# Optimization experiments

Hardware: AMD Instinct MI355X
Metric: run time of the kernel (lower is better)

Reference implementation:

```python
import jax, jax.numpy as jnp
import numpy as np

IN_CH = 4
OUT_CH = 64
T = 100            # max points per pillar
P_MAX = 12000      # max pillars
DX = 0.16
DY = 0.16
XMIN, YMIN, ZMIN, XMAX, YMAX, ZMAX = -40.0, -40.0, -3.0, 40.0, 40.0, 1.0
NX = int(round((XMAX - XMIN) / DX))   # 500
NY = int(round((YMAX - YMIN) / DY))   # 500
EPS = 1e-5
B, N = 2, 120000


def setup_inputs() -> dict:
    key = jax.random.key(0)
    ks = jax.random.split(key, 8)
    # realistic LiDAR-like cloud: x,y spread over the grid, z mostly in range
    xy = jax.random.normal(ks[0], (B, N, 2)) * 15.0
    z = jax.random.uniform(ks[1], (B, N, 1), minval=-3.2, maxval=1.2)
    inten = jax.random.uniform(ks[2], (B, N, 1))
    points = jnp.concatenate([xy, z, inten], axis=-1)

    def bn_params(k):
        k1, k2, k3, k4 = jax.random.split(k, 4)
        g = 1.0 + 0.1 * jax.random.normal(k1, (OUT_CH,))
        b = 0.1 * jax.random.normal(k2, (OUT_CH,))
        m = 0.1 * jax.random.normal(k3, (OUT_CH,))
        v = 0.5 + jax.random.uniform(k4, (OUT_CH,))
        return g, b, m, v

    w1 = jax.random.normal(ks[3], (OUT_CH, IN_CH + 4)) * 0.3
    w2 = jax.random.normal(ks[4], (OUT_CH, OUT_CH)) * 0.1
    g1, b1, m1, v1 = bn_params(ks[5])
    g2, b2, m2, v2 = bn_params(ks[6])
    return dict(points=points, w1=w1, g1=g1, b1=b1, m1=m1, v1=v1,
                w2=w2, g2=g2, b2=b2, m2=m2, v2=v2)


def _pillarize(pts):
    # pts: [N, 4] -> dense pillar tensor [P_MAX, T, 8], validity mask, pillar keys
    x, y, z = pts[:, 0], pts[:, 1], pts[:, 2]
    valid = (x >= XMIN) & (x < XMAX) & (y >= YMIN) & (y < YMAX) & (z >= ZMIN) & (z < ZMAX)
    xi = jnp.clip(jnp.floor((x - XMIN) / DX), 0, NX - 1).astype(jnp.int32)
    yi = jnp.clip(jnp.floor((y - YMIN) / DY), 0, NY - 1).astype(jnp.int32)
    big = jnp.int32(NX * NY)  # sentinel key for invalid points (sorts last)
    keyv = jnp.where(valid, xi * NY + yi, big)
    order = jnp.argsort(keyv)          # stable sort == torch.unique ordering
    sk = keyv[order]
    ps = pts[order]
    vs = sk < big
    n = pts.shape[0]
    idx = jnp.arange(n, dtype=jnp.int32)
    new = vs & jnp.concatenate([jnp.ones((1,), bool), sk[1:] != sk[:-1]])
    rank = jnp.cumsum(new.astype(jnp.int32)) - 1          # dense pillar id (sorted)
    p_eff = jnp.minimum(jnp.sum(new.astype(jnp.int32)), P_MAX)
    start = jax.lax.cummax(jnp.where(new, idx, jnp.int32(-1)))
    intra = idx - start                                   # slot within pillar
    keep = vs & (rank < P_MAX) & (intra < T)
    r = jnp.where(keep, rank, P_MAX)
    t = jnp.where(keep, intra, T)
    pillar_pts = jnp.zeros((P_MAX, T, IN_CH), pts.dtype).at[r, t].set(ps, mode='drop')
    keys = jnp.zeros((P_MAX,), jnp.int32).at[r].set(sk, mode='drop')
    pvalid = jnp.arange(P_MAX, dtype=jnp.int32) < p_eff
    xi_u = (keys // NY).astype(pts.dtype)
    yi_u = (keys % NY).astype(pts.dtype)
    xc = xi_u * DX + XMIN + DX / 2
    yc = yi_u * DY + YMIN + DY / 2
    # enhanced features are computed for ALL T slots (incl. empty), like the original
    x_off = pillar_pts[:, :, 0] - xc[:, None]
    y_off = pillar_pts[:, :, 1] - yc[:, None]
    xc_t = jnp.broadcast_to(xc[:, None], (P_MAX, T))
    yc_t = jnp.broadcast_to(yc[:, None], (P_MAX, T))
    enh = jnp.stack([xc_t, yc_t, x_off, y_off], axis=-1)
    pin = jnp.concatenate([pillar_pts, enh], axis=-1)     # [P_MAX, T, 8]
    return pin, pvalid, keys


def _forward(points, w1, g1, b1, m1, v1, w2, g2, b2, m2, v2):
    pin, pvalid, keys = jax.vmap(_pillarize)(points)      # [B, P_MAX, T, 8]

    def bn(h, g, b, m, v):
        return (h - m) * (g * jax.lax.rsqrt(v + EPS)) + b

    h = jax.nn.relu(bn(jnp.einsum('bptc,oc->bpto', pin, w1), g1, b1, m1, v1))
    h = jax.nn.relu(bn(jnp.einsum('bptc,oc->bpto', h, w2), g2, b2, m2, v2))
    feats = jnp.max(h, axis=2)                            # max-pool over T
    feats = jnp.where(pvalid[..., None], feats, 0.0)      # zero-pad unused pillars
    bidx = jnp.broadcast_to(jnp.arange(points.shape[0], dtype=jnp.int32)[:, None], pvalid.shape)
    xi_u = jnp.where(pvalid, keys // NY, 0)
    yi_u = jnp.where(pvalid, keys % NY, 0)
    coords = jnp.stack([bidx, xi_u, yi_u], axis=-1)       # [B, P_MAX, 3]
    return feats, coords


def reference(points, w1, g1, b1, m1, v1, w2, g2, b2, m2, v2):
    return _forward(points, w1, g1, b1, m1, v1, w2, g2, b2, m2, v2)
```

## Files before the change

kernel.cpp:

```cpp
#include <hip/hip_runtime.h>
#include <stdint.h>
#include <stddef.h>

#define NBATCH 2
#define NPTS   120000
#define T_SLOTS 100
#define PMAX   12000
#define NXG    500
#define NYG    500
#define NBINS  (NXG*NYG)
#define NCH    ((NBINS + 63)/64)
#define NG     ((NCH + 63)/64)

#define FEAT_BLOCKS 6000

#define WS_FLAGS   ((size_t)0)
#define WS_SLOT    (WS_FLAGS + (size_t)NBATCH*NBINS)
#define WS_ZEROEND (WS_SLOT  + (size_t)NBATCH*PMAX*4)
#define WS_MASKS   (WS_ZEROEND)
#define WS_PDAT    (WS_MASKS + (size_t)NBATCH*NCH*8)
#define WS_CHOFF   (WS_PDAT  + (size_t)NBATCH*PMAX*T_SLOTS*16)
#define WS_PILKEY  (WS_CHOFF + (size_t)NBATCH*NCH*4)
#define WS_GRPS    (WS_PILKEY+ (size_t)NBATCH*PMAX*4)
#define WS_PTOT    (WS_GRPS  + (size_t)NBATCH*NG*4)
#define WS_NEEDED  (WS_PTOT  + (size_t)NBATCH*4)

#define ZERO_F4    (WS_ZEROEND / 16)


__global__ void k_zero(float4* __restrict__ dst) {
    int i = blockIdx.x * blockDim.x + threadIdx.x;
    if (i < (int)ZERO_F4) {
        float4 z; z.x = 0.0f; z.y = 0.0f; z.z = 0.0f; z.w = 0.0f;
        dst[i] = z;
    }
}

__global__ void k_key(const float4* __restrict__ pts4,
                      unsigned char* __restrict__ flags) {
    int i = blockIdx.x * blockDim.x + threadIdx.x;
    if (i >= NBATCH * NPTS) return;
    int b = i / NPTS;
    float4 P = pts4[i];
    float x = P.x, y = P.y, z = P.z;
    bool valid = (x >= -40.0f) && (x < 40.0f) &&
                 (y >= -40.0f) && (y < 40.0f) &&
                 (z >= -3.0f)  && (z < 1.0f);
    if (valid) {
        float fx = floorf((x + 40.0f) / 0.16f);
        float fy = floorf((y + 40.0f) / 0.16f);
        fx = fminf(fmaxf(fx, 0.0f), (float)(NXG - 1));
        fy = fminf(fmaxf(fy, 0.0f), (float)(NYG - 1));
        int key = (int)fx * NYG + (int)fy;
        flags[(size_t)b * NBINS + key] = 1;
    }
}

__global__ __launch_bounds__(1024)
void k_scanA(const unsigned char* __restrict__ flags,
             unsigned long long* __restrict__ masks,
             int* __restrict__ grpsum) {
    __shared__ int scnt[64];
    const int g    = blockIdx.x;
    const int b    = blockIdx.y;
    const int tid  = threadIdx.x;
    const int lane = tid & 63;
    const int w    = tid >> 6;
    const unsigned char* fb = flags + (size_t)b * NBINS;

    #pragma unroll
    for (int q = 0; q < 4; ++q) {
        int chl = w * 4 + q;
        int ch  = g * 64 + chl;
        int bin = ch * 64 + lane;
        int pres = (ch < NCH && bin < NBINS && fb[bin]) ? 1 : 0;
        unsigned long long m = __ballot(pres);
        if (lane == 0) {
            if (ch < NCH) masks[(size_t)b * NCH + ch] = m;
            scnt[chl] = __popcll(m);
        }
    }
    __syncthreads();
    if (w == 0) {
        int v = scnt[lane];
        #pragma unroll
        for (int off = 32; off > 0; off >>= 1) v += __shfl_xor(v, off);
        if (lane == 0) grpsum[b * NG + g] = v;
    }
}

__global__ void k_choff(const unsigned long long* __restrict__ masks,
                        const int* __restrict__ grpsum,
                        int* __restrict__ choff, int* __restrict__ ptot) {
    int tid  = threadIdx.x;
    int lane = tid & 63;
    int gw   = blockIdx.x * 4 + (tid >> 6);
    if (gw >= NBATCH * NG) return;
    int b = gw / NG, g = gw - b * NG;

    int gs = (lane < NG) ? grpsum[b * NG + lane] : 0;
    int incl = gs;
    #pragma unroll
    for (int off = 1; off < 64; off <<= 1) {
        int t2 = __shfl_up(incl, off);
        if (lane >= off) incl += t2;
    }
    int tot  = __shfl(incl, NG - 1);
    int goff = __shfl(incl, (g == 0) ? 0 : g - 1);
    if (g == 0) goff = 0;
    if (g == 0 && lane == 0) ptot[b] = tot;

    int ch = g * 64 + lane;
    int cs = (ch < NCH) ? __popcll(masks[(size_t)b * NCH + ch]) : 0;
    int incl2 = cs;
    #pragma unroll
    for (int off = 1; off < 64; off <<= 1) {
        int t2 = __shfl_up(incl2, off);
        if (lane >= off) incl2 += t2;
    }
    if (ch < NCH) choff[(size_t)b * NCH + ch] = goff + incl2 - cs;
}

__global__ void k_fill(const float4* __restrict__ pts4,
                       const unsigned long long* __restrict__ masks,
                       const int* __restrict__ choff, int* __restrict__ slotctr,
                       int* __restrict__ pilkey, float4* __restrict__ pdat) {
    int i = blockIdx.x * blockDim.x + threadIdx.x;
    if (i >= NBATCH * NPTS) return;
    int b = i / NPTS;
    float4 P = pts4[i];
    float x = P.x, y = P.y, z = P.z;
    bool valid = (x >= -40.0f) && (x < 40.0f) &&
                 (y >= -40.0f) && (y < 40.0f) &&
                 (z >= -3.0f)  && (z < 1.0f);
    if (!valid) return;
    float fx = floorf((x + 40.0f) / 0.16f);
    float fy = floorf((y + 40.0f) / 0.16f);
    fx = fminf(fmaxf(fx, 0.0f), (float)(NXG - 1));
    fy = fminf(fmaxf(fy, 0.0f), (float)(NYG - 1));
    int key = (int)fx * NYG + (int)fy;

    int ch = key >> 6;
    unsigned long long m = masks[(size_t)b * NCH + ch];
    int r = choff[(size_t)b * NCH + ch] +
            __popcll(m & ((1ULL << (key & 63)) - 1ULL));
    if (r >= PMAX) return;
    pilkey[b * PMAX + r] = key;
    int t = atomicAdd(&slotctr[b * PMAX + r], 1);
    if (t < T_SLOTS)
        pdat[((size_t)(b * PMAX + r)) * T_SLOTS + t] = P;
}

__global__ __launch_bounds__(256, 8)
void k_feats(const float4* __restrict__ pdat,
             const float* __restrict__ w1, const float* __restrict__ g1,
             const float* __restrict__ b1, const float* __restrict__ m1,
             const float* __restrict__ v1,
             const float* __restrict__ w2, const float* __restrict__ g2,
             const float* __restrict__ b2, const float* __restrict__ m2,
             const float* __restrict__ v2,
             const int* __restrict__ pilkey, const int* __restrict__ slotctr,
             const int* __restrict__ ptot, float* __restrict__ out) {
    __shared__ float4 w2s[16 * 64];
    __shared__ __align__(16) float h1s[4][64];

    const int tid  = threadIdx.x;
    const int lane = tid & 63;
    const int widx = tid >> 6;
    const int o = lane;

    float* feats  = out;
    float* coords = out + (size_t)NBATCH * PMAX * 64;

    const int p = blockIdx.x * 4 + widx;
    const int b = p / PMAX;
    const int r = p - b * PMAX;

    const float4* prow = pdat + (size_t)p * T_SLOTS;
    int key = pilkey[p];
    int c   = slotctr[p];
    int pe = ptot[b]; if (pe > PMAX) pe = PMAX;

    float s1 = g1[o] * rsqrtf(v1[o] + 1e-5f);
    float b1f = b1[o] - m1[o] * s1;
    float w1r[8];
    {
        const float4* w14 = (const float4*)(w1 + o * 8);
        float4 a = w14[0], c4 = w14[1];
        w1r[0] = a.x * s1;  w1r[1] = a.y * s1;  w1r[2] = a.z * s1;  w1r[3] = a.w * s1;
        w1r[4] = c4.x * s1; w1r[5] = c4.y * s1; w1r[6] = c4.z * s1; w1r[7] = c4.w * s1;
    }
    float wx = w1r[0] + w1r[6];
    float wy = w1r[1] + w1r[7];

    float s2 = g2[o] * rsqrtf(v2[o] + 1e-5f);
    float b2f = b2[o] - m2[o] * s2;
    {
        const float4* w2row = (const float4*)(w2 + o * 64);
        #pragma unroll
        for (int it = 0; it < 4; ++it) {
            int kq = widx + it * 4;
            float4 t = w2row[kq];
            t.x *= s2; t.y *= s2; t.z *= s2; t.w *= s2;
            w2s[kq * 64 + o] = t;
        }
    }
    __syncthreads();

    size_t frow = (size_t)p * 64;
    size_t crow = (size_t)p * 3;

    if (r >= pe) {
        feats[frow + o] = 0.0f;
        if (o < 3) coords[crow + o] = (o == 0) ? (float)b : 0.0f;
        return;
    }

    int xi = key / NYG;
    int yi = key - xi * NYG;
    float xc = (float)xi * 0.16f - 40.0f + 0.08f;
    float yc = (float)yi * 0.16f - 40.0f + 0.08f;

    float pb = b1f + (w1r[4] - w1r[6]) * xc + (w1r[5] - w1r[7]) * yc;

    int pc = (c < T_SLOTS) ? c : T_SLOTS;
    int nIter = pc + ((c < T_SLOTS) ? 1 : 0);

    float acc = 0.0f;
    for (int s = 0; s < nIter; ++s) {
        float4 P;
        if (s < pc) {
            P = prow[s];
        } else {
            P.x = 0.0f; P.y = 0.0f; P.z = 0.0f; P.w = 0.0f;
        }
        float h = pb;
        h += wx * P.x; h += wy * P.y;
        h += w1r[2] * P.z; h += w1r[3] * P.w;
        h = fmaxf(h, 0.0f);

        h1s[widx][o] = h;
        asm volatile("s_waitcnt lgkmcnt(0)" ::: "memory");

        float a0 = b2f, a1 = 0.0f, a2 = 0.0f, a3 = 0.0f;
        #pragma unroll
        for (int kq = 0; kq < 16; ++kq) {
            float4 w  = w2s[kq * 64 + o];
            float4 hb = *(const float4*)&h1s[widx][kq * 4];
            a0 += w.x * hb.x; a1 += w.y * hb.y;
            a2 += w.z * hb.z; a3 += w.w * hb.w;
        }
        float h2 = fmaxf((a0 + a1) + (a2 + a3), 0.0f);
        acc = fmaxf(acc, h2);
    }

    feats[frow + o] = acc;
    if (o < 3)
        coords[crow + o] = (o == 0) ? (float)b : ((o == 1) ? (float)xi : (float)yi);
}


extern "C" void kernel_launch(void* const* d_in, const int* in_sizes, int n_in,
                              void* d_out, int out_size, void* d_ws, size_t ws_size,
                              hipStream_t stream) {
    if (ws_size < WS_NEEDED) return;

    const float4* pts4 = (const float4*)d_in[0];
    const float* w1  = (const float*)d_in[1];
    const float* g1  = (const float*)d_in[2];
    const float* b1  = (const float*)d_in[3];
    const float* m1  = (const float*)d_in[4];
    const float* v1  = (const float*)d_in[5];
    const float* w2  = (const float*)d_in[6];
    const float* g2  = (const float*)d_in[7];
    const float* b2  = (const float*)d_in[8];
    const float* m2  = (const float*)d_in[9];
    const float* v2  = (const float*)d_in[10];

    char* ws = (char*)d_ws;
    unsigned char* flags = (unsigned char*)(ws + WS_FLAGS);
    int*  slotctr = (int*)(ws + WS_SLOT);
    unsigned long long* masks = (unsigned long long*)(ws + WS_MASKS);
    float4* pdat  = (float4*)(ws + WS_PDAT);
    int*  choff   = (int*)(ws + WS_CHOFF);
    int*  pilkey  = (int*)(ws + WS_PILKEY);
    int*  grpsum  = (int*)(ws + WS_GRPS);
    int*  ptot    = (int*)(ws + WS_PTOT);
    float* out    = (float*)d_out;

    dim3 blk256(256);
    int npt = NBATCH * NPTS;
    dim3 grdPts((npt + 255) / 256);

    hipLaunchKernelGGL(k_zero, dim3((ZERO_F4 + 255) / 256), blk256, 0, stream,
                       (float4*)(ws + WS_FLAGS));

    hipLaunchKernelGGL(k_key, grdPts, blk256, 0, stream, pts4, flags);

    hipLaunchKernelGGL(k_scanA, dim3(NG, NBATCH), dim3(1024), 0, stream,
                       flags, masks, grpsum);

    hipLaunchKernelGGL(k_choff, dim3((NBATCH * NG + 3) / 4), blk256, 0, stream,
                       masks, grpsum, choff, ptot);

    hipLaunchKernelGGL(k_fill, grdPts, blk256, 0, stream,
                       pts4, masks, choff, slotctr, pilkey, pdat);

    hipLaunchKernelGGL(k_feats, dim3(FEAT_BLOCKS), blk256, 0, stream,
                       pdat, w1, g1, b1, m1, v1, w2, g2, b2, m2, v2,
                       pilkey, slotctr, ptot, out);
}
```

Before: 48.16 us.

## Process two batch pillars per wavefront to reuse shared weight loads

Each wavefront now handles pillar r from both batches at once. Every w2 row read from shared memory is reused for two hidden vectors, and half as many blocks are launched, so each block's weight setup in LDS is paid once per pair of pillars. The cost is loop divergence when the two pillars have different point counts, extra registers, and the dot product regrouped into two accumulators instead of four, which lengthens the dependency chains.

```diff
diff --git a/kernel.cpp b/kernel.cpp
--- a/kernel.cpp
+++ b/kernel.cpp
@@ -12,7 +12,7 @@
 #define NCH    ((NBINS + 63)/64)
 #define NG     ((NCH + 63)/64)
 
-#define FEAT_BLOCKS 6000
+#define FEAT_BLOCKS 3000
 
 #define WS_FLAGS   ((size_t)0)
 #define WS_SLOT    (WS_FLAGS + (size_t)NBATCH*NBINS)
@@ -162,7 +162,7 @@
              const int* __restrict__ pilkey, const int* __restrict__ slotctr,
              const int* __restrict__ ptot, float* __restrict__ out) {
     __shared__ float4 w2s[16 * 64];
-    __shared__ __align__(16) float h1s[4][64];
+    __shared__ __align__(16) float h1s[4][2][64];
 
     const int tid  = threadIdx.x;
     const int lane = tid & 63;
@@ -172,14 +172,16 @@
     float* feats  = out;
     float* coords = out + (size_t)NBATCH * PMAX * 64;
 
-    const int p = blockIdx.x * 4 + widx;
-    const int b = p / PMAX;
-    const int r = p - b * PMAX;
-
-    const float4* prow = pdat + (size_t)p * T_SLOTS;
-    int key = pilkey[p];
-    int c   = slotctr[p];
-    int pe = ptot[b]; if (pe > PMAX) pe = PMAX;
+    const int r  = blockIdx.x * 4 + widx;
+    const int pA = r;
+    const int pB = r + PMAX;
+
+    const float4* prowA = pdat + (size_t)pA * T_SLOTS;
+    const float4* prowB = pdat + (size_t)pB * T_SLOTS;
+    int keyA = pilkey[pA], keyB = pilkey[pB];
+    int cA   = slotctr[pA], cB = slotctr[pB];
+    int pe0 = ptot[0]; if (pe0 > PMAX) pe0 = PMAX;
+    int pe1 = ptot[1]; if (pe1 > PMAX) pe1 = PMAX;
 
     float s1 = g1[o] * rsqrtf(v1[o] + 1e-5f);
     float b1f = b1[o] - m1[o] * s1;
@@ -207,56 +209,71 @@
     }
     __syncthreads();
 
-    size_t frow = (size_t)p * 64;
-    size_t crow = (size_t)p * 3;
-
-    if (r >= pe) {
-        feats[frow + o] = 0.0f;
-        if (o < 3) coords[crow + o] = (o == 0) ? (float)b : 0.0f;
-        return;
-    }
-
-    int xi = key / NYG;
-    int yi = key - xi * NYG;
-    float xc = (float)xi * 0.16f - 40.0f + 0.08f;
-    float yc = (float)yi * 0.16f - 40.0f + 0.08f;
-
-    float pb = b1f + (w1r[4] - w1r[6]) * xc + (w1r[5] - w1r[7]) * yc;
-
-    int pc = (c < T_SLOTS) ? c : T_SLOTS;
-    int nIter = pc + ((c < T_SLOTS) ? 1 : 0);
-
-    float acc = 0.0f;
-    for (int s = 0; s < nIter; ++s) {
-        float4 P;
-        if (s < pc) {
-            P = prow[s];
-        } else {
-            P.x = 0.0f; P.y = 0.0f; P.z = 0.0f; P.w = 0.0f;
-        }
-        float h = pb;
-        h += wx * P.x; h += wy * P.y;
-        h += w1r[2] * P.z; h += w1r[3] * P.w;
-        h = fmaxf(h, 0.0f);
-
-        h1s[widx][o] = h;
+    int xiA = keyA / NYG, yiA = keyA - xiA * NYG;
+    int xiB = keyB / NYG, yiB = keyB - xiB * NYG;
+    float xcA = (float)xiA * 0.16f - 40.0f + 0.08f;
+    float ycA = (float)yiA * 0.16f - 40.0f + 0.08f;
+    float xcB = (float)xiB * 0.16f - 40.0f + 0.08f;
+    float ycB = (float)yiB * 0.16f - 40.0f + 0.08f;
+    float pbA = b1f + (w1r[4] - w1r[6]) * xcA + (w1r[5] - w1r[7]) * ycA;
+    float pbB = b1f + (w1r[4] - w1r[6]) * xcB + (w1r[5] - w1r[7]) * ycB;
+
+    bool liveA = (r < pe0), liveB = (r < pe1);
+    int pcA = liveA ? ((cA < T_SLOTS) ? cA : T_SLOTS) : 0;
+    int pcB = liveB ? ((cB < T_SLOTS) ? cB : T_SLOTS) : 0;
+    int nItA = liveA ? (pcA + ((cA < T_SLOTS) ? 1 : 0)) : 0;
+    int nItB = liveB ? (pcB + ((cB < T_SLOTS) ? 1 : 0)) : 0;
+    int maxN = (nItA > nItB) ? nItA : nItB;
+
+    float accA = 0.0f, accB = 0.0f;
+
+    for (int s = 0; s < maxN; ++s) {
+        float4 PA, PB;
+        if (s < pcA) PA = prowA[s];
+        else { PA.x = 0.0f; PA.y = 0.0f; PA.z = 0.0f; PA.w = 0.0f; }
+        if (s < pcB) PB = prowB[s];
+        else { PB.x = 0.0f; PB.y = 0.0f; PB.z = 0.0f; PB.w = 0.0f; }
+
+        float hA = pbA;
+        hA += wx * PA.x; hA += wy * PA.y;
+        hA += w1r[2] * PA.z; hA += w1r[3] * PA.w;
+        hA = fmaxf(hA, 0.0f);
+        float hB = pbB;
+        hB += wx * PB.x; hB += wy * PB.y;
+        hB += w1r[2] * PB.z; hB += w1r[3] * PB.w;
+        hB = fmaxf(hB, 0.0f);
+
+        h1s[widx][0][o] = hA;
+        h1s[widx][1][o] = hB;
         asm volatile("s_waitcnt lgkmcnt(0)" ::: "memory");
 
-        float a0 = b2f, a1 = 0.0f, a2 = 0.0f, a3 = 0.0f;
+        float aA0 = b2f, aA1 = 0.0f, aB0 = b2f, aB1 = 0.0f;
         #pragma unroll
         for (int kq = 0; kq < 16; ++kq) {
             float4 w  = w2s[kq * 64 + o];
-            float4 hb = *(const float4*)&h1s[widx][kq * 4];
-            a0 += w.x * hb.x; a1 += w.y * hb.y;
-            a2 += w.z * hb.z; a3 += w.w * hb.w;
+            float4 qA = *(const float4*)&h1s[widx][0][kq * 4];
+            float4 qB = *(const float4*)&h1s[widx][1][kq * 4];
+            aA0 += w.x * qA.x; aA1 += w.y * qA.y;
+            aA0 += w.z * qA.z; aA1 += w.w * qA.w;
+            aB0 += w.x * qB.x; aB1 += w.y * qB.y;
+            aB0 += w.z * qB.z; aB1 += w.w * qB.w;
         }
-        float h2 = fmaxf((a0 + a1) + (a2 + a3), 0.0f);
-        acc = fmaxf(acc, h2);
-    }
-
-    feats[frow + o] = acc;
-    if (o < 3)
-        coords[crow + o] = (o == 0) ? (float)b : ((o == 1) ? (float)xi : (float)yi);
+        if (s < nItA) accA = fmaxf(accA, fmaxf(aA0 + aA1, 0.0f));
+        if (s < nItB) accB = fmaxf(accB, fmaxf(aB0 + aB1, 0.0f));
+    }
+
+    size_t frowA = (size_t)pA * 64, crowA = (size_t)pA * 3;
+    size_t frowB = (size_t)pB * 64, crowB = (size_t)pB * 3;
+    feats[frowA + o] = liveA ? accA : 0.0f;
+    feats[frowB + o] = liveB ? accB : 0.0f;
+    if (o < 3) {
+        coords[crowA + o] = liveA
+            ? ((o == 0) ? 0.0f : (o == 1) ? (float)xiA : (float)yiA)
+            : 0.0f;
+        coords[crowB + o] = liveB
+            ? ((o == 0) ? 1.0f : (o == 1) ? (float)xiB : (float)yiB)
+            : ((o == 0) ? 1.0f : 0.0f);
+    }
 }
 
 
```

Measured after the change: 43.17 us (median of 2 runs). 1.12x faster.
